# Kernel optimization log

Measured on AMD Instinct MI355X. Metric: run time of the kernel, lower is better.

The kernel has to match this reference:

```python
import jax, jax.numpy as jnp
import numpy as np

N, E, D_NODE, D_EDGE, H, NUM_CLASSES = 2048, 4096, 128, 128, 4, 16
SPARSE_RATIO = 0.5  # forward arg sparse_ratio; <1.0 triggers top-k node masking
NEG = jnp.float32(-1e9)


def _mha(x, wq, bq, wk, bk, wv, bv, wo, bo, mask):
    """Multi-head self-attention over tokens x [T, D]; mask broadcastable to [H, T, T]."""
    T, D = x.shape
    dh = D // H
    q = (x @ wq + bq).reshape(T, H, dh)
    k = (x @ wk + bk).reshape(T, H, dh)
    v = (x @ wv + bv).reshape(T, H, dh)
    scores = jnp.einsum('qhd,khd->hqk', q, k) * (1.0 / float(np.sqrt(dh)))
    scores = jnp.where(mask, scores, NEG)
    attn = jax.nn.softmax(scores, axis=-1)
    out = jnp.einsum('hqk,khd->qhd', attn, v).reshape(T, D)
    return out @ wo + bo


def setup_inputs() -> dict:
    key = jax.random.key(0)
    ks = jax.random.split(key, 20)
    f32 = jnp.float32
    def w(i, shape):
        return jax.random.normal(ks[i], shape, dtype=f32) * 0.02
    z = lambda *s: jnp.zeros(s, f32)
    return {
        'node_features': jax.random.normal(ks[0], (N, D_NODE), dtype=f32),
        'edge_features': jax.random.normal(ks[1], (E, D_EDGE), dtype=f32),
        'edge_index': jax.random.randint(ks[2], (2, E), 0, N),
        'w_rn': w(3, (D_NODE, 1)), 'b_rn': z(1),
        'w_re': w(4, (D_EDGE, 1)), 'b_re': z(1),
        'wq_n': w(5, (D_NODE, D_NODE)), 'bq_n': z(D_NODE),
        'wk_n': w(6, (D_NODE, D_NODE)), 'bk_n': z(D_NODE),
        'wv_n': w(7, (D_NODE, D_NODE)), 'bv_n': z(D_NODE),
        'wo_n': w(8, (D_NODE, D_NODE)), 'bo_n': z(D_NODE),
        'wq_e': w(9, (D_EDGE, D_EDGE)), 'bq_e': z(D_EDGE),
        'wk_e': w(10, (D_EDGE, D_EDGE)), 'bk_e': z(D_EDGE),
        'wv_e': w(11, (D_EDGE, D_EDGE)), 'bv_e': z(D_EDGE),
        'wo_e': w(12, (D_EDGE, D_EDGE)), 'bo_e': z(D_EDGE),
        'w_ne': w(13, (D_NODE, D_EDGE)), 'b_ne': z(D_EDGE),
        'w_c1': w(14, (D_EDGE, 2 * D_EDGE)), 'b_c1': z(2 * D_EDGE),
        'w_c2': w(15, (2 * D_EDGE, NUM_CLASSES)), 'b_c2': z(NUM_CLASSES),
    }


def reference(node_features, edge_features, edge_index,
              w_rn, b_rn, w_re, b_re,
              wq_n, bq_n, wk_n, bk_n, wv_n, bv_n, wo_n, bo_n,
              wq_e, bq_e, wk_e, bk_e, wv_e, bv_e, wo_e, bo_e,
              w_ne, b_ne, w_c1, b_c1, w_c2, b_c2):
    # Importance router: scalar sigmoid scores per node / edge
    node_scores = jax.nn.sigmoid(node_features @ w_rn + b_rn)[:, 0]  # [N]
    edge_scores = jax.nn.sigmoid(edge_features @ w_re + b_re)[:, 0]  # [E]
    # Gate features by importance (routing)
    x_n = node_features * node_scores[:, None]
    x_e = edge_features * edge_scores[:, None]
    # Conditional top-k node mask (sparse_ratio < 1.0)
    k = int(SPARSE_RATIO * N)
    thresh = jax.lax.top_k(node_scores, k)[0][-1]
    node_mask = node_scores >= thresh  # [N] bool, keys kept in node attention
    # Edge adjacency (line graph): edges sharing an endpoint attend to each other
    src, dst = edge_index[0], edge_index[1]
    adj = ((src[:, None] == src[None, :]) | (src[:, None] == dst[None, :]) |
           (dst[:, None] == src[None, :]) | (dst[:, None] == dst[None, :]))  # [E, E]
    # Dual parallel attention
    node_out = _mha(x_n, wq_n, bq_n, wk_n, bk_n, wv_n, bv_n, wo_n, bo_n,
                    node_mask[None, None, :])
    edge_out = _mha(x_e, wq_e, bq_e, wk_e, bk_e, wv_e, bv_e, wo_e, bo_e,
                    adj[None, :, :])
    node_msg = node_out[src] + node_out[dst]  # [E, D_NODE] gather at endpoints
    updated_edges = edge_out + node_msg @ w_ne + b_ne  # [E, D_EDGE]
    # Classifier: Linear -> GELU -> Linear
    h = jax.nn.gelu(updated_edges @ w_c1 + b_c1)
    return h @ w_c2 + b_c2  # [E, NUM_CLASSES]
```

## Files before the change

### kernel.cpp

```cpp
#include <hip/hip_runtime.h>
#include <math.h>

#define N_NODES 2048
#define N_EDGES 4096
#define DIM 128
#define HEADS 4
#define DH 32
#define NCLS 16
#define TOPK 1024
#define NBR_CAP 64
#define NSPLIT 4
#define QB 32
#define SCALE 0.17677669529663687f

#define FMA4(ACC, AS, BV)                                       \
  ACC.x = fmaf(AS, BV.x, ACC.x); ACC.y = fmaf(AS, BV.y, ACC.y); \
  ACC.z = fmaf(AS, BV.z, ACC.z); ACC.w = fmaf(AS, BV.w, ACC.w)

__device__ __forceinline__ float wave_reduce_sum(float v) {
#pragma unroll
  for (int o = 32; o > 0; o >>= 1) v += __shfl_xor(v, o, 64);
  return v;
}

__global__ __launch_bounds__(256) void prep_kernel(
    const float* __restrict__ nf, const float* __restrict__ ef,
    const float* __restrict__ w_rn, const float* __restrict__ b_rn,
    const float* __restrict__ w_re, const float* __restrict__ b_re,
    const int* __restrict__ src, const int* __restrict__ dst,
    const float* __restrict__ wo_n, const float* __restrict__ bo_n,
    const float* __restrict__ w_ne, const float* __restrict__ b_ne,
    float* __restrict__ ns, float* __restrict__ es, int* __restrict__ nbr,
    int* __restrict__ deg, float* __restrict__ wfu, float* __restrict__ bfu) {
  int tid = threadIdx.x;
  int bid = blockIdx.x;
  if (bid < 1536) {
    int wid = tid >> 6, lane = tid & 63;
    int row = bid * 4 + wid;
    const float* feat;
    const float* w;
    float b;
    float* scp;
    if (row < N_NODES) {
      feat = nf + (size_t)row * DIM;
      w = w_rn; b = b_rn[0];
      scp = ns + row;
    } else {
      int r = row - N_NODES;
      feat = ef + (size_t)r * DIM;
      w = w_re; b = b_re[0];
      scp = es + r;
    }
    float d = feat[lane] * w[lane] + feat[lane + 64] * w[lane + 64];
    d = wave_reduce_sum(d);
    if (lane == 0) *scp = 1.0f / (1.0f + __expf(-(d + b)));
    return;
  }
  if (bid < 2048) {
    __shared__ int sL[N_EDGES];
    __shared__ int dL[N_EDGES];
    __shared__ int cnt[8];
    int bq = bid - 1536;
#pragma unroll
    for (int i = 0; i < 16; i++) {
      int j = i * 256 + tid;
      sL[j] = src[j];
      dL[j] = dst[j];
    }
    if (tid < 8) cnt[tid] = 0;
    __syncthreads();
    int w = tid >> 6, lane = tid & 63;
#pragma unroll
    for (int qq = 0; qq < 2; qq++) {
      int slot = w * 2 + qq;
      int qi = bq * 8 + slot;
      int sq = sL[qi], dq = dL[qi];
      for (int j = lane; j < N_EDGES; j += 64) {
        int sj = sL[j], dj = dL[j];
        if (sj == sq || sj == dq || dj == sq || dj == dq) {
          int pos = atomicAdd(&cnt[slot], 1);
          if (pos < NBR_CAP) nbr[(size_t)qi * NBR_CAP + pos] = j;
        }
      }
    }
    __syncthreads();
    if (tid < 8) deg[bq * 8 + tid] = min(cnt[tid], NBR_CAP);
    return;
  }
  if (bid < 2052) {
    __shared__ float As[16][68];
    __shared__ float Bs[16][68];
    int idx = bid - 2048;
    int bm = (idx >> 1) * 64, bn = (idx & 1) * 64;
    int tm = (tid >> 4) * 4, tn = (tid & 15) * 4;
    float4 acc[4] = {{0,0,0,0},{0,0,0,0},{0,0,0,0},{0,0,0,0}};
    for (int k0 = 0; k0 < DIM; k0 += 16) {
#pragma unroll
      for (int i = 0; i < 4; i++) {
        int e = i * 256 + tid;
        int r = e >> 4, kk = e & 15;
        As[kk][r] = wo_n[(size_t)(bm + r) * DIM + k0 + kk];
        int kb = e >> 6, c = e & 63;
        Bs[kb][c] = w_ne[(size_t)(k0 + kb) * DIM + bn + c];
      }
      __syncthreads();
#pragma unroll
      for (int kk = 0; kk < 16; kk++) {
        float4 a = *(const float4*)&As[kk][tm];
        float4 b = *(const float4*)&Bs[kk][tn];
        FMA4(acc[0], a.x, b); FMA4(acc[1], a.y, b);
        FMA4(acc[2], a.z, b); FMA4(acc[3], a.w, b);
      }
      __syncthreads();
    }
#pragma unroll
    for (int i = 0; i < 4; i++)
      *(float4*)&wfu[(size_t)(bm + tm + i) * DIM + bn + tn] = acc[i];
    return;
  }
  if (tid < DIM) {
    float a = 0.f;
    for (int k = 0; k < DIM; k++)
      a = fmaf(bo_n[k], w_ne[(size_t)k * DIM + tid], a);
    bfu[tid] = 2.f * a + b_ne[tid];
  }
}

typedef float As128T[16][136];
typedef float Bs68T[16][68];
__device__ __forceinline__ void gemm_body128(
    As128T& As, Bs68T& Bs, const float* __restrict__ A,
    const float* __restrict__ B, const float* gs, int bm, int bn, int K,
    int N, float4 (&acc)[8], int tid) {
  int g4 = (tid >> 4) * 4, tn = (tid & 15) * 4;
  for (int k0 = 0; k0 < K; k0 += 16) {
#pragma unroll
    for (int i = 0; i < 8; i++) {
      int e = i * 256 + tid;
      int r = e >> 4, kk = e & 15;
      float a = A[(size_t)(bm + r) * K + k0 + kk];
      As[kk][r] = gs ? a * gs[r] : a;
    }
#pragma unroll
    for (int i = 0; i < 4; i++) {
      int e = i * 256 + tid;
      int kb = e >> 6, c = e & 63;
      Bs[kb][c] = B[(size_t)(k0 + kb) * N + bn + c];
    }
    __syncthreads();
#pragma unroll
    for (int kk = 0; kk < 16; kk++) {
      float4 a0 = *(const float4*)&As[kk][g4];
      float4 a1 = *(const float4*)&As[kk][g4 + 64];
      float4 b = *(const float4*)&Bs[kk][tn];
      FMA4(acc[0], a0.x, b); FMA4(acc[1], a0.y, b);
      FMA4(acc[2], a0.z, b); FMA4(acc[3], a0.w, b);
      FMA4(acc[4], a1.x, b); FMA4(acc[5], a1.y, b);
      FMA4(acc[6], a1.z, b); FMA4(acc[7], a1.w, b);
    }
    __syncthreads();
  }
}

__global__ __launch_bounds__(256) void topk_qkv_kernel(
    const float* __restrict__ nf, const float* __restrict__ ef,
    const float* __restrict__ ns, const float* __restrict__ es,
    const float* __restrict__ wq_n, const float* __restrict__ wk_n,
    const float* __restrict__ wv_n, const float* __restrict__ wq_e,
    const float* __restrict__ wk_e, const float* __restrict__ wv_e,
    const float* __restrict__ bq_n, const float* __restrict__ bk_n,
    const float* __restrict__ bv_n, const float* __restrict__ bq_e,
    const float* __restrict__ bk_e, const float* __restrict__ bv_e,
    float* __restrict__ qn, float* __restrict__ kn, float* __restrict__ vn,
    float* __restrict__ qe, float* __restrict__ ke, float* __restrict__ ve,
    int* __restrict__ kidx, int* __restrict__ nkept) {
  __shared__ float As[16][136];
  __shared__ float Bs[16][68];
  __shared__ float ss[128];
  __shared__ unsigned sh_lo;
  __shared__ int wcnt;
  int tid = threadIdx.x;
  if (blockIdx.x == 0) {
    if (tid == 0) wcnt = 0;
    if (tid < 64) {
      unsigned bv[32];
#pragma unroll
      for (int i = 0; i < 32; i++) bv[i] = __float_as_uint(ns[tid * 32 + i]);
      unsigned lo = 0u, hi = 0x3F800000u;
      while (lo < hi) {
        unsigned mid = (unsigned)(((unsigned long long)lo + hi + 1ull) >> 1);
        int c = 0;
#pragma unroll
        for (int i = 0; i < 32; i++) c += (bv[i] >= mid);
#pragma unroll
        for (int o = 1; o < 64; o <<= 1) c += __shfl_xor(c, o, 64);
        if (c >= TOPK) lo = mid; else hi = mid - 1;
      }
      if (tid == 0) sh_lo = lo;
    }
    __syncthreads();
    unsigned lo = sh_lo;
#pragma unroll
    for (int i = 0; i < 8; i++) {
      int idx = tid * 8 + i;
      if (__float_as_uint(ns[idx]) >= lo) kidx[atomicAdd(&wcnt, 1)] = idx;
    }
    __syncthreads();
    if (tid == 0) nkept[0] = wcnt;
    return;
  }
  int bx = blockIdx.x - 1;
  bool edge = bx >= 96;
  int mat, bm, bn;
  const float* A;
  const float* sc;
  if (!edge) {
    mat = bx / 32;
    int rem = bx % 32;
    bm = (rem >> 1) * 128;
    bn = (rem & 1) * 64;
    A = nf; sc = ns;
  } else {
    int be = bx - 96;
    mat = be / 64;
    int rem = be % 64;
    bm = (rem >> 1) * 128;
    bn = (rem & 1) * 64;
    A = ef; sc = es;
  }
  const float* W;
  const float* bias;
  float* C;
  if (!edge) {
    if (mat == 0) { W = wq_n; bias = bq_n; C = qn; }
    else if (mat == 1) { W = wk_n; bias = bk_n; C = kn; }
    else { W = wv_n; bias = bv_n; C = vn; }
  } else {
    if (mat == 0) { W = wq_e; bias = bq_e; C = qe; }
    else if (mat == 1) { W = wk_e; bias = bk_e; C = ke; }
    else { W = wv_e; bias = bv_e; C = ve; }
  }
  if (tid < 128) ss[tid] = sc[bm + tid];
  __syncthreads();
  float4 acc[8] = {{0,0,0,0},{0,0,0,0},{0,0,0,0},{0,0,0,0},
                   {0,0,0,0},{0,0,0,0},{0,0,0,0},{0,0,0,0}};
  gemm_body128(As, Bs, A, W, ss, bm, bn, DIM, DIM, acc, tid);
  int g4 = (tid >> 4) * 4, tn = (tid & 15) * 4;
  float4 b4 = *(const float4*)&bias[bn + tn];
#pragma unroll
  for (int i = 0; i < 4; i++) {
    float4 r;
    r.x = acc[i].x + b4.x; r.y = acc[i].y + b4.y;
    r.z = acc[i].z + b4.z; r.w = acc[i].w + b4.w;
    *(float4*)&C[(size_t)(bm + g4 + i) * DIM + bn + tn] = r;
  }
#pragma unroll
  for (int i = 0; i < 4; i++) {
    float4 r;
    r.x = acc[4 + i].x + b4.x; r.y = acc[4 + i].y + b4.y;
    r.z = acc[4 + i].z + b4.z; r.w = acc[4 + i].w + b4.w;
    *(float4*)&C[(size_t)(bm + 64 + g4 + i) * DIM + bn + tn] = r;
  }
}

__global__ __launch_bounds__(256) void attn_kernel(
    const float* __restrict__ Q, const float* __restrict__ K,
    const float* __restrict__ V, const int* __restrict__ kidx,
    const int* __restrict__ nkeptp, float* __restrict__ pacc,
    float* __restrict__ ps,
    const float* __restrict__ Qe, const float* __restrict__ Ke,
    const float* __restrict__ Ve, const int* __restrict__ nbr,
    const int* __restrict__ deg, float* __restrict__ Oe) {
  __shared__ float Qs[32][36];
  __shared__ float Ks[64][36];
  __shared__ float Vs[64][36];
  __shared__ float Ps[32][68];
  int tid = threadIdx.x;
  int bid = blockIdx.x;
  if (bid < 1024) {
    int bxa = bid & 63;
    int h = (bid >> 6) & 3;
    int sp = bid >> 8;
    int qbase = bxa * QB;
    int nkept = nkeptp[0];
    int spl = (nkept + NSPLIT - 1) / NSPLIT;
    int start = sp * spl;
    int end = min(start + spl, nkept);

    {
      int q8 = tid >> 3, d8 = tid & 7;
      const float4* qp =
          (const float4*)(Q + (size_t)(qbase + q8) * DIM + h * DH) + d8;
      float4 qv = *qp;
      Qs[d8 * 4 + 0][q8] = qv.x;
      Qs[d8 * 4 + 1][q8] = qv.y;
      Qs[d8 * 4 + 2][q8] = qv.z;
      Qs[d8 * 4 + 3][q8] = qv.w;
    }

    int tq = tid >> 5;
    int tk = tid & 31;
    float o[4] = {0.f, 0.f, 0.f, 0.f};
    float sump[4] = {0.f, 0.f, 0.f, 0.f};

    for (int t0 = start; t0 < end; t0 += 64) {
#pragma unroll
      for (int i = 0; i < 2; i++) {
        int id = i * 256 + tid;
        int r = id >> 3, c4 = id & 7;
        int row = t0 + r;
        int ki = (row < end) ? kidx[row] : kidx[0];
        const float4* kp = (const float4*)(K + (size_t)ki * DIM + h * DH) + c4;
        const float4* vp = (const float4*)(V + (size_t)ki * DIM + h * DH) + c4;
        *(float4*)&Ks[r][c4 * 4] = *kp;
        *(float4*)&Vs[r][c4 * 4] = *vp;
      }
      __syncthreads();
      float4 s0v = {0.f, 0.f, 0.f, 0.f};
      float4 s1v = {0.f, 0.f, 0.f, 0.f};
#pragma unroll
      for (int kk4 = 0; kk4 < 8; kk4++) {
        int kk = kk4 * 4;
        float4 ka = *(const float4*)&Ks[tk][kk];
        float4 kb = *(const float4*)&Ks[tk + 32][kk];
        float4 qa = *(const float4*)&Qs[kk + 0][tq * 4];
        float4 qb = *(const float4*)&Qs[kk + 1][tq * 4];
        float4 qc = *(const float4*)&Qs[kk + 2][tq * 4];
        float4 qd = *(const float4*)&Qs[kk + 3][tq * 4];
        FMA4(s0v, ka.x, qa); FMA4(s0v, ka.y, qb);
        FMA4(s0v, ka.z, qc); FMA4(s0v, ka.w, qd);
        FMA4(s1v, kb.x, qa); FMA4(s1v, kb.y, qb);
        FMA4(s1v, kb.z, qc); FMA4(s1v, kb.w, qd);
      }
      bool va = (t0 + tk) < end;
      bool vb = (t0 + tk + 32) < end;
      float p00 = va ? __expf(s0v.x * SCALE) : 0.f;
      float p01 = va ? __expf(s0v.y * SCALE) : 0.f;
      float p02 = va ? __expf(s0v.z * SCALE) : 0.f;
      float p03 = va ? __expf(s0v.w * SCALE) : 0.f;
      float p10 = vb ? __expf(s1v.x * SCALE) : 0.f;
      float p11 = vb ? __expf(s1v.y * SCALE) : 0.f;
      float p12 = vb ? __expf(s1v.z * SCALE) : 0.f;
      float p13 = vb ? __expf(s1v.w * SCALE) : 0.f;
      Ps[tq * 4 + 0][tk] = p00;      Ps[tq * 4 + 1][tk] = p01;
      Ps[tq * 4 + 2][tk] = p02;      Ps[tq * 4 + 3][tk] = p03;
      Ps[tq * 4 + 0][tk + 32] = p10; Ps[tq * 4 + 1][tk + 32] = p11;
      Ps[tq * 4 + 2][tk + 32] = p12; Ps[tq * 4 + 3][tk + 32] = p13;
      sump[0] += p00 + p10;
      sump[1] += p01 + p11;
      sump[2] += p02 + p12;
      sump[3] += p03 + p13;
      __syncthreads();
#pragma unroll
      for (int k4 = 0; k4 < 16; k4++) {
        int k = k4 * 4;
        float4 p0 = *(const float4*)&Ps[tq * 4 + 0][k];
        float4 p1 = *(const float4*)&Ps[tq * 4 + 1][k];
        float4 p2 = *(const float4*)&Ps[tq * 4 + 2][k];
        float4 p3 = *(const float4*)&Ps[tq * 4 + 3][k];
        float w0 = Vs[k + 0][tk], w1 = Vs[k + 1][tk];
        float w2 = Vs[k + 2][tk], w3 = Vs[k + 3][tk];
        o[0] = fmaf(p0.x, w0, o[0]); o[0] = fmaf(p0.y, w1, o[0]);
        o[0] = fmaf(p0.z, w2, o[0]); o[0] = fmaf(p0.w, w3, o[0]);
        o[1] = fmaf(p1.x, w0, o[1]); o[1] = fmaf(p1.y, w1, o[1]);
        o[1] = fmaf(p1.z, w2, o[1]); o[1] = fmaf(p1.w, w3, o[1]);
        o[2] = fmaf(p2.x, w0, o[2]); o[2] = fmaf(p2.y, w1, o[2]);
        o[2] = fmaf(p2.z, w2, o[2]); o[2] = fmaf(p2.w, w3, o[2]);
        o[3] = fmaf(p3.x, w0, o[3]); o[3] = fmaf(p3.y, w1, o[3]);
        o[3] = fmaf(p3.z, w2, o[3]); o[3] = fmaf(p3.w, w3, o[3]);
      }
      __syncthreads();
    }
#pragma unroll
    for (int os = 1; os < 32; os <<= 1) {
#pragma unroll
      for (int j = 0; j < 4; j++) sump[j] += __shfl_xor(sump[j], os, 64);
    }
#pragma unroll
    for (int j = 0; j < 4; j++) {
      int q = qbase + tq * 4 + j;
      size_t idx = ((size_t)q * HEADS + h) * NSPLIT + sp;
      pacc[idx * 32 + tk] = o[j];
      if (tk == 0) ps[idx] = sump[j];
    }
    return;
  }
  int h = tid >> 6;
  int lane = tid & 63;
  int ql = lane >> 4, j4 = (lane >> 2) & 3, g = lane & 3;
  int qi = (bid - 1024) * 4 + ql;
  int dg = deg[qi];
  const float4* qp = (const float4*)(Qe + (size_t)qi * DIM + h * DH + g * 8);
  float4 q0 = qp[0], q1 = qp[1];
  float s = 0.f;
  float4 a0 = make_float4(0.f, 0.f, 0.f, 0.f);
  float4 a1 = make_float4(0.f, 0.f, 0.f, 0.f);
  for (int c0 = 0; c0 < dg; c0 += 4) {
    int j = c0 + j4;
    bool act = j < dg;
    int ei = act ? nbr[(size_t)qi * NBR_CAP + j] : 0;
    const float4* kp = (const float4*)(Ke + (size_t)ei * DIM + h * DH + g * 8);
    float4 k0 = kp[0], k1 = kp[1];
    float pd = q0.x * k0.x + q0.y * k0.y + q0.z * k0.z + q0.w * k0.w +
               q1.x * k1.x + q1.y * k1.y + q1.z * k1.z + q1.w * k1.w;
    pd += __shfl_xor(pd, 1, 64);
    pd += __shfl_xor(pd, 2, 64);
    float pr = act ? __expf(pd * SCALE) : 0.f;
    s += pr;
    const float4* vp = (const float4*)(Ve + (size_t)ei * DIM + h * DH + g * 8);
    float4 v0 = vp[0], v1 = vp[1];
    FMA4(a0, pr, v0);
    FMA4(a1, pr, v1);
  }
#pragma unroll
  for (int o = 4; o <= 8; o <<= 1) {
    s += __shfl_xor(s, o, 64);
    a0.x += __shfl_xor(a0.x, o, 64); a0.y += __shfl_xor(a0.y, o, 64);
    a0.z += __shfl_xor(a0.z, o, 64); a0.w += __shfl_xor(a0.w, o, 64);
    a1.x += __shfl_xor(a1.x, o, 64); a1.y += __shfl_xor(a1.y, o, 64);
    a1.z += __shfl_xor(a1.z, o, 64); a1.w += __shfl_xor(a1.w, o, 64);
  }
  if (j4 == 0) {
    float inv = 1.0f / s;
    float4* op = (float4*)(Oe + (size_t)qi * DIM + h * DH + g * 8);
    float4 r0 = {a0.x * inv, a0.y * inv, a0.z * inv, a0.w * inv};
    float4 r1 = {a1.x * inv, a1.y * inv, a1.z * inv, a1.w * inv};
    op[0] = r0;
    op[1] = r1;
  }
}

__global__ __launch_bounds__(256) void attn_reduce_kernel(
    const float* __restrict__ pacc, const float* __restrict__ ps,
    float* __restrict__ O) {
  int gid = blockIdx.x * 256 + threadIdx.x;
  int qh = gid >> 5, d = gid & 31;
  int q = qh >> 2, h = qh & 3;
  float ssum = 0.f, v = 0.f;
#pragma unroll
  for (int sp = 0; sp < NSPLIT; sp++) {
    size_t idx = (size_t)qh * NSPLIT + sp;
    ssum += ps[idx];
    v += pacc[idx * 32 + d];
  }
  O[(size_t)q * DIM + h * DH + d] = v / ssum;
}

__global__ __launch_bounds__(256) void tail_kernel(
    const float* __restrict__ aoe, const float* __restrict__ wo_e,
    const float* __restrict__ bo_e, const float* __restrict__ aon,
    const int* __restrict__ src, const int* __restrict__ dst,
    const float* __restrict__ wfu, const float* __restrict__ bfu,
    const float* __restrict__ w_c1, const float* __restrict__ b_c1,
    float* __restrict__ hb) {
  __shared__ __align__(16) char smem[25344];
  float (*ue_s)[132] = (float(*)[132])smem;
  float (*As0)[20] = (float(*)[20])(smem + 8448);
  float (*Bs)[132] = (float(*)[132])(smem + 9728);
  float (*Bs2)[264] = (float(*)[264])(smem + 8448);
  int tid = threadIdx.x;
  int bm = blockIdx.x * 16;
  int tmr = (tid >> 5) * 2;
  int tn = (tid & 31) * 4;
  float4 acc[2] = {{0,0,0,0},{0,0,0,0}};
  for (int k0 = 0; k0 < DIM; k0 += 16) {
    {
      int r = tid >> 4, kk = tid & 15;
      As0[kk][r] = aoe[(size_t)(bm + r) * DIM + k0 + kk];
    }
#pragma unroll
    for (int i = 0; i < 8; i++) {
      int id = i * 256 + tid;
      int kb = id >> 7, c = id & 127;
      Bs[kb][c] = wo_e[(size_t)(k0 + kb) * DIM + c];
    }
    __syncthreads();
#pragma unroll
    for (int kk = 0; kk < 16; kk++) {
      float2 a = *(const float2*)&As0[kk][tmr];
      float4 b = *(const float4*)&Bs[kk][tn];
      FMA4(acc[0], a.x, b);
      FMA4(acc[1], a.y, b);
    }
    __syncthreads();
  }
  for (int k0 = 0; k0 < DIM; k0 += 16) {
    {
      int r = tid >> 4, kk = tid & 15;
      int row = bm + r;
      int s0 = src[row], d0 = dst[row];
      As0[kk][r] = aon[(size_t)s0 * DIM + k0 + kk] +
                   aon[(size_t)d0 * DIM + k0 + kk];
    }
#pragma unroll
    for (int i = 0; i < 8; i++) {
      int id = i * 256 + tid;
      int kb = id >> 7, c = id & 127;
      Bs[kb][c] = wfu[(size_t)(k0 + kb) * DIM + c];
    }
    __syncthreads();
#pragma unroll
    for (int kk = 0; kk < 16; kk++) {
      float2 a = *(const float2*)&As0[kk][tmr];
      float4 b = *(const float4*)&Bs[kk][tn];
      FMA4(acc[0], a.x, b);
      FMA4(acc[1], a.y, b);
    }
    __syncthreads();
  }
  {
    float4 be = *(const float4*)&bo_e[tn];
    float4 bf = *(const float4*)&bfu[tn];
#pragma unroll
    for (int i = 0; i < 2; i++) {
      float4 r;
      r.x = acc[i].x + be.x + bf.x; r.y = acc[i].y + be.y + bf.y;
      r.z = acc[i].z + be.z + bf.z; r.w = acc[i].w + be.w + bf.w;
      *(float4*)&ue_s[tmr + i][tn] = r;
    }
  }
  __syncthreads();
  int c4 = (tid & 31) * 4;
  float4 acc2[2][2] = {{{0,0,0,0},{0,0,0,0}},{{0,0,0,0},{0,0,0,0}}};
  for (int k0 = 0; k0 < DIM; k0 += 16) {
#pragma unroll
    for (int i = 0; i < 16; i++) {
      int id = i * 256 + tid;
      int kb = id >> 8, c = id & 255;
      Bs2[kb][c] = w_c1[(size_t)(k0 + kb) * 256 + c];
    }
    __syncthreads();
#pragma unroll
    for (int kk = 0; kk < 16; kk++) {
      float a0v = ue_s[tmr][k0 + kk];
      float a1v = ue_s[tmr + 1][k0 + kk];
      float4 bva = *(const float4*)&Bs2[kk][c4];
      float4 bvb = *(const float4*)&Bs2[kk][c4 + 128];
      FMA4(acc2[0][0], a0v, bva); FMA4(acc2[0][1], a0v, bvb);
      FMA4(acc2[1][0], a1v, bva); FMA4(acc2[1][1], a1v, bvb);
    }
    __syncthreads();
  }
  float4 bc0 = *(const float4*)&b_c1[c4];
  float4 bc1 = *(const float4*)&b_c1[c4 + 128];
#pragma unroll
  for (int i = 0; i < 2; i++) {
#pragma unroll
    for (int half = 0; half < 2; half++) {
      float4 bb = half ? bc1 : bc0;
      float vv[4] = {acc2[i][half].x + bb.x, acc2[i][half].y + bb.y,
                     acc2[i][half].z + bb.z, acc2[i][half].w + bb.w};
#pragma unroll
      for (int j = 0; j < 4; j++) {
        float v = vv[j];
        float u = 0.7978845608028654f * (v + 0.044715f * v * v * v);
        vv[j] = 0.5f * v * (1.0f + tanhf(u));
      }
      float4 r = {vv[0], vv[1], vv[2], vv[3]};
      *(float4*)&hb[(size_t)(bm + tmr + i) * 256 + c4 + half * 128] = r;
    }
  }
}

__global__ __launch_bounds__(256) void gemm_out_kernel(
    const float* __restrict__ Hm, const float* __restrict__ B,
    const float* __restrict__ bias, float* __restrict__ C) {
  __shared__ float Bs[256 * 16];
  int tid = threadIdx.x;
#pragma unroll
  for (int i = 0; i < 16; i++) Bs[i * 256 + tid] = B[i * 256 + tid];
  __syncthreads();
  int row = blockIdx.x * 16 + (tid >> 4);
  int col = tid & 15;
  const float* hp = Hm + (size_t)row * 256;
  float sacc = bias[col];
#pragma unroll 8
  for (int k = 0; k < 256; k++) sacc = fmaf(hp[k], Bs[k * 16 + col], sacc);
  C[(size_t)row * NCLS + col] = sacc;
}

extern "C" void kernel_launch(void* const* d_in, const int* in_sizes, int n_in,
                              void* d_out, int out_size, void* d_ws,
                              size_t ws_size, hipStream_t stream) {
  const float* nf = (const float*)d_in[0];
  const float* ef = (const float*)d_in[1];
  const int* ei = (const int*)d_in[2];
  const float* w_rn = (const float*)d_in[3];
  const float* b_rn = (const float*)d_in[4];
  const float* w_re = (const float*)d_in[5];
  const float* b_re = (const float*)d_in[6];
  const float* wq_n = (const float*)d_in[7];
  const float* bq_n = (const float*)d_in[8];
  const float* wk_n = (const float*)d_in[9];
  const float* bk_n = (const float*)d_in[10];
  const float* wv_n = (const float*)d_in[11];
  const float* bv_n = (const float*)d_in[12];
  const float* wo_n = (const float*)d_in[13];
  const float* bo_n = (const float*)d_in[14];
  const float* wq_e = (const float*)d_in[15];
  const float* bq_e = (const float*)d_in[16];
  const float* wk_e = (const float*)d_in[17];
  const float* bk_e = (const float*)d_in[18];
  const float* wv_e = (const float*)d_in[19];
  const float* bv_e = (const float*)d_in[20];
  const float* wo_e = (const float*)d_in[21];
  const float* bo_e = (const float*)d_in[22];
  const float* w_ne = (const float*)d_in[23];
  const float* b_ne = (const float*)d_in[24];
  const float* w_c1 = (const float*)d_in[25];
  const float* b_c1 = (const float*)d_in[26];
  const float* w_c2 = (const float*)d_in[27];
  const float* b_c2 = (const float*)d_in[28];

  const int* src = ei;
  const int* dst = ei + N_EDGES;

  float* ws = (float*)d_ws;
  size_t o = 0;
  float* ns = ws + o;   o += 2048;
  float* es = ws + o;   o += 4096;
  int* kidx = (int*)(ws + o); o += 2048;
  int* nkept = (int*)(ws + o); o += 64;
  int* nbr = (int*)(ws + o); o += (size_t)N_EDGES * NBR_CAP;
  int* degp = (int*)(ws + o); o += N_EDGES;
  float* wfu = ws + o;  o += DIM * DIM;
  float* bfu = ws + o;  o += DIM;
  float* qn = ws + o;   o += (size_t)N_NODES * DIM;
  float* kn = ws + o;   o += (size_t)N_NODES * DIM;
  float* vn = ws + o;   o += (size_t)N_NODES * DIM;
  float* qe = ws + o;   o += (size_t)N_EDGES * DIM;
  float* ke = ws + o;   o += (size_t)N_EDGES * DIM;
  float* ve = ws + o;   o += (size_t)N_EDGES * DIM;
  float* aon = ws + o;  o += (size_t)N_NODES * DIM;
  float* aoe = ws + o;  o += (size_t)N_EDGES * DIM;
  float* hb = ws + o;   o += (size_t)N_EDGES * 2 * DIM;
  float* ps = ws + o;   o += (size_t)N_NODES * HEADS * NSPLIT;
  float* pacc = hb;

  prep_kernel<<<dim3(2053), 256, 0, stream>>>(
      nf, ef, w_rn, b_rn, w_re, b_re, src, dst, wo_n, bo_n, w_ne, b_ne,
      ns, es, nbr, degp, wfu, bfu);
  topk_qkv_kernel<<<dim3(289), 256, 0, stream>>>(
      nf, ef, ns, es, wq_n, wk_n, wv_n, wq_e, wk_e, wv_e,
      bq_n, bk_n, bv_n, bq_e, bk_e, bv_e, qn, kn, vn, qe, ke, ve,
      kidx, nkept);
  attn_kernel<<<dim3(2048), 256, 0, stream>>>(
      qn, kn, vn, kidx, nkept, pacc, ps, qe, ke, ve, nbr, degp, aoe);
  attn_reduce_kernel<<<dim3(N_NODES * HEADS * DH / 256), 256, 0, stream>>>(
      pacc, ps, aon);
  tail_kernel<<<dim3(N_EDGES / 16), 256, 0, stream>>>(
      aoe, wo_e, bo_e, aon, src, dst, wfu, bfu, w_c1, b_c1, hb);
  gemm_out_kernel<<<dim3(N_EDGES / 16), 256, 0, stream>>>(hb, w_c2, b_c2,
                                                          (float*)d_out);
}
```

Measured before the change: 115.3 us.

## Increase block counts and split work in neighbor build, attention PV, tail, output GEMM

The line-graph neighbor builder now handles 4 query edges per block instead of 8, doubling its block count. The node attention P·V step splits the key dimension across four thread groups with float4 V reads, then reduces the partial outputs through shared memory. The tail and output GEMM kernels process 8 rows per block instead of 16, and the output GEMM splits K across two halves with a shared-memory reduction. All of this aims to raise parallelism and occupancy, at the cost of extra syncs, reductions and redundant loads of src/dst and weights.

```diff
diff --git a/kernel.cpp b/kernel.cpp
--- a/kernel.cpp
+++ b/kernel.cpp
@@ -56,10 +56,10 @@
     if (lane == 0) *scp = 1.0f / (1.0f + __expf(-(d + b)));
     return;
   }
-  if (bid < 2048) {
+  if (bid < 2560) {
     __shared__ int sL[N_EDGES];
     __shared__ int dL[N_EDGES];
-    __shared__ int cnt[8];
+    __shared__ int cnt[4];
     int bq = bid - 1536;
 #pragma unroll
     for (int i = 0; i < 16; i++) {
@@ -67,30 +67,26 @@
       sL[j] = src[j];
       dL[j] = dst[j];
     }
-    if (tid < 8) cnt[tid] = 0;
+    if (tid < 4) cnt[tid] = 0;
     __syncthreads();
     int w = tid >> 6, lane = tid & 63;
-#pragma unroll
-    for (int qq = 0; qq < 2; qq++) {
-      int slot = w * 2 + qq;
-      int qi = bq * 8 + slot;
-      int sq = sL[qi], dq = dL[qi];
-      for (int j = lane; j < N_EDGES; j += 64) {
-        int sj = sL[j], dj = dL[j];
-        if (sj == sq || sj == dq || dj == sq || dj == dq) {
-          int pos = atomicAdd(&cnt[slot], 1);
-          if (pos < NBR_CAP) nbr[(size_t)qi * NBR_CAP + pos] = j;
-        }
-      }
-    }
-    __syncthreads();
-    if (tid < 8) deg[bq * 8 + tid] = min(cnt[tid], NBR_CAP);
+    int qi = bq * 4 + w;
+    int sq = sL[qi], dq = dL[qi];
+    for (int j = lane; j < N_EDGES; j += 64) {
+      int sj = sL[j], dj = dL[j];
+      if (sj == sq || sj == dq || dj == sq || dj == dq) {
+        int pos = atomicAdd(&cnt[w], 1);
+        if (pos < NBR_CAP) nbr[(size_t)qi * NBR_CAP + pos] = j;
+      }
+    }
+    __syncthreads();
+    if (tid < 4) deg[bq * 4 + tid] = min(cnt[tid], NBR_CAP);
     return;
   }
-  if (bid < 2052) {
+  if (bid < 2564) {
     __shared__ float As[16][68];
     __shared__ float Bs[16][68];
-    int idx = bid - 2048;
+    int idx = bid - 2560;
     int bm = (idx >> 1) * 64, bn = (idx & 1) * 64;
     int tm = (tid >> 4) * 4, tn = (tid & 15) * 4;
     float4 acc[4] = {{0,0,0,0},{0,0,0,0},{0,0,0,0},{0,0,0,0}};
@@ -300,7 +296,10 @@
 
     int tq = tid >> 5;
     int tk = tid & 31;
-    float o[4] = {0.f, 0.f, 0.f, 0.f};
+    int kg = tid >> 6;
+    int tq2 = (tid >> 3) & 7;
+    int td4 = tid & 7;
+    float4 o4[4] = {{0,0,0,0},{0,0,0,0},{0,0,0,0},{0,0,0,0}};
     float sump[4] = {0.f, 0.f, 0.f, 0.f};
 
     for (int t0 = start; t0 < end; t0 += 64) {
@@ -352,22 +351,24 @@
       sump[3] += p03 + p13;
       __syncthreads();
 #pragma unroll
-      for (int k4 = 0; k4 < 16; k4++) {
-        int k = k4 * 4;
-        float4 p0 = *(const float4*)&Ps[tq * 4 + 0][k];
-        float4 p1 = *(const float4*)&Ps[tq * 4 + 1][k];
-        float4 p2 = *(const float4*)&Ps[tq * 4 + 2][k];
-        float4 p3 = *(const float4*)&Ps[tq * 4 + 3][k];
-        float w0 = Vs[k + 0][tk], w1 = Vs[k + 1][tk];
-        float w2 = Vs[k + 2][tk], w3 = Vs[k + 3][tk];
-        o[0] = fmaf(p0.x, w0, o[0]); o[0] = fmaf(p0.y, w1, o[0]);
-        o[0] = fmaf(p0.z, w2, o[0]); o[0] = fmaf(p0.w, w3, o[0]);
-        o[1] = fmaf(p1.x, w0, o[1]); o[1] = fmaf(p1.y, w1, o[1]);
-        o[1] = fmaf(p1.z, w2, o[1]); o[1] = fmaf(p1.w, w3, o[1]);
-        o[2] = fmaf(p2.x, w0, o[2]); o[2] = fmaf(p2.y, w1, o[2]);
-        o[2] = fmaf(p2.z, w2, o[2]); o[2] = fmaf(p2.w, w3, o[2]);
-        o[3] = fmaf(p3.x, w0, o[3]); o[3] = fmaf(p3.y, w1, o[3]);
-        o[3] = fmaf(p3.z, w2, o[3]); o[3] = fmaf(p3.w, w3, o[3]);
+      for (int k4 = 0; k4 < 4; k4++) {
+        int kb = kg * 16 + k4 * 4;
+        float4 p0 = *(const float4*)&Ps[tq2 * 4 + 0][kb];
+        float4 p1 = *(const float4*)&Ps[tq2 * 4 + 1][kb];
+        float4 p2 = *(const float4*)&Ps[tq2 * 4 + 2][kb];
+        float4 p3 = *(const float4*)&Ps[tq2 * 4 + 3][kb];
+        float4 v0 = *(const float4*)&Vs[kb + 0][td4 * 4];
+        float4 v1 = *(const float4*)&Vs[kb + 1][td4 * 4];
+        float4 v2 = *(const float4*)&Vs[kb + 2][td4 * 4];
+        float4 v3 = *(const float4*)&Vs[kb + 3][td4 * 4];
+        FMA4(o4[0], p0.x, v0); FMA4(o4[0], p0.y, v1);
+        FMA4(o4[0], p0.z, v2); FMA4(o4[0], p0.w, v3);
+        FMA4(o4[1], p1.x, v0); FMA4(o4[1], p1.y, v1);
+        FMA4(o4[1], p1.z, v2); FMA4(o4[1], p1.w, v3);
+        FMA4(o4[2], p2.x, v0); FMA4(o4[2], p2.y, v1);
+        FMA4(o4[2], p2.z, v2); FMA4(o4[2], p2.w, v3);
+        FMA4(o4[3], p3.x, v0); FMA4(o4[3], p3.y, v1);
+        FMA4(o4[3], p3.z, v2); FMA4(o4[3], p3.w, v3);
       }
       __syncthreads();
     }
@@ -376,12 +377,37 @@
 #pragma unroll
       for (int j = 0; j < 4; j++) sump[j] += __shfl_xor(sump[j], os, 64);
     }
-#pragma unroll
-    for (int j = 0; j < 4; j++) {
-      int q = qbase + tq * 4 + j;
-      size_t idx = ((size_t)q * HEADS + h) * NSPLIT + sp;
-      pacc[idx * 32 + tk] = o[j];
-      if (tk == 0) ps[idx] = sump[j];
+    if (tk == 0) {
+#pragma unroll
+      for (int j = 0; j < 4; j++) {
+        int q = qbase + tq * 4 + j;
+        size_t idx = ((size_t)q * HEADS + h) * NSPLIT + sp;
+        ps[idx] = sump[j];
+      }
+    }
+    float* scrA = &Ks[0][0];
+    float* scrB = &Vs[0][0];
+    int slot = (kg * 64 + tq2 * 8 + td4) * 8;
+    *(float4*)&scrA[slot + 0] = o4[0];
+    *(float4*)&scrA[slot + 4] = o4[1];
+    *(float4*)&scrB[slot + 0] = o4[2];
+    *(float4*)&scrB[slot + 4] = o4[3];
+    __syncthreads();
+    {
+      int qq = tid >> 3;
+      int d4 = tid & 7;
+      int tqr = qq >> 2, j = qq & 3;
+      const float* bank = (j < 2) ? scrA : scrB;
+      int off = (j & 1) * 4;
+      float4 of = {0.f, 0.f, 0.f, 0.f};
+#pragma unroll
+      for (int g = 0; g < 4; g++) {
+        float4 part =
+            *(const float4*)&bank[(g * 64 + tqr * 8 + d4) * 8 + off];
+        of.x += part.x; of.y += part.y; of.z += part.z; of.w += part.w;
+      }
+      size_t idx = ((size_t)(qbase + qq) * HEADS + h) * NSPLIT + sp;
+      *(float4*)&pacc[idx * 32 + d4 * 4] = of;
     }
     return;
   }
@@ -453,18 +479,18 @@
     const float* __restrict__ wfu, const float* __restrict__ bfu,
     const float* __restrict__ w_c1, const float* __restrict__ b_c1,
     float* __restrict__ hb) {
-  __shared__ __align__(16) char smem[25344];
+  __shared__ __align__(16) char smem[21120];
   float (*ue_s)[132] = (float(*)[132])smem;
-  float (*As0)[20] = (float(*)[20])(smem + 8448);
-  float (*Bs)[132] = (float(*)[132])(smem + 9728);
-  float (*Bs2)[264] = (float(*)[264])(smem + 8448);
+  float (*As0)[12] = (float(*)[12])(smem + 4224);
+  float (*Bs)[132] = (float(*)[132])(smem + 4992);
+  float (*Bs2)[264] = (float(*)[264])(smem + 4224);
   int tid = threadIdx.x;
-  int bm = blockIdx.x * 16;
-  int tmr = (tid >> 5) * 2;
+  int bm = blockIdx.x * 8;
+  int tr = tid >> 5;
   int tn = (tid & 31) * 4;
-  float4 acc[2] = {{0,0,0,0},{0,0,0,0}};
+  float4 acc = {0, 0, 0, 0};
   for (int k0 = 0; k0 < DIM; k0 += 16) {
-    {
+    if (tid < 128) {
       int r = tid >> 4, kk = tid & 15;
       As0[kk][r] = aoe[(size_t)(bm + r) * DIM + k0 + kk];
     }
@@ -477,15 +503,14 @@
     __syncthreads();
 #pragma unroll
     for (int kk = 0; kk < 16; kk++) {
-      float2 a = *(const float2*)&As0[kk][tmr];
+      float a = As0[kk][tr];
       float4 b = *(const float4*)&Bs[kk][tn];
-      FMA4(acc[0], a.x, b);
-      FMA4(acc[1], a.y, b);
+      FMA4(acc, a, b);
     }
     __syncthreads();
   }
   for (int k0 = 0; k0 < DIM; k0 += 16) {
-    {
+    if (tid < 128) {
       int r = tid >> 4, kk = tid & 15;
       int row = bm + r;
       int s0 = src[row], d0 = dst[row];
@@ -501,27 +526,23 @@
     __syncthreads();
 #pragma unroll
     for (int kk = 0; kk < 16; kk++) {
-      float2 a = *(const float2*)&As0[kk][tmr];
+      float a = As0[kk][tr];
       float4 b = *(const float4*)&Bs[kk][tn];
-      FMA4(acc[0], a.x, b);
-      FMA4(acc[1], a.y, b);
+      FMA4(acc, a, b);
     }
     __syncthreads();
   }
   {
     float4 be = *(const float4*)&bo_e[tn];
     float4 bf = *(const float4*)&bfu[tn];
-#pragma unroll
-    for (int i = 0; i < 2; i++) {
-      float4 r;
-      r.x = acc[i].x + be.x + bf.x; r.y = acc[i].y + be.y + bf.y;
-      r.z = acc[i].z + be.z + bf.z; r.w = acc[i].w + be.w + bf.w;
-      *(float4*)&ue_s[tmr + i][tn] = r;
-    }
+    float4 r;
+    r.x = acc.x + be.x + bf.x; r.y = acc.y + be.y + bf.y;
+    r.z = acc.z + be.z + bf.z; r.w = acc.w + be.w + bf.w;
+    *(float4*)&ue_s[tr][tn] = r;
   }
   __syncthreads();
   int c4 = (tid & 31) * 4;
-  float4 acc2[2][2] = {{{0,0,0,0},{0,0,0,0}},{{0,0,0,0},{0,0,0,0}}};
+  float4 acc2[2] = {{0,0,0,0},{0,0,0,0}};
   for (int k0 = 0; k0 < DIM; k0 += 16) {
 #pragma unroll
     for (int i = 0; i < 16; i++) {
@@ -532,33 +553,29 @@
     __syncthreads();
 #pragma unroll
     for (int kk = 0; kk < 16; kk++) {
-      float a0v = ue_s[tmr][k0 + kk];
-      float a1v = ue_s[tmr + 1][k0 + kk];
+      float av = ue_s[tr][k0 + kk];
       float4 bva = *(const float4*)&Bs2[kk][c4];
       float4 bvb = *(const float4*)&Bs2[kk][c4 + 128];
-      FMA4(acc2[0][0], a0v, bva); FMA4(acc2[0][1], a0v, bvb);
-      FMA4(acc2[1][0], a1v, bva); FMA4(acc2[1][1], a1v, bvb);
+      FMA4(acc2[0], av, bva);
+      FMA4(acc2[1], av, bvb);
     }
     __syncthreads();
   }
   float4 bc0 = *(const float4*)&b_c1[c4];
   float4 bc1 = *(const float4*)&b_c1[c4 + 128];
 #pragma unroll
-  for (int i = 0; i < 2; i++) {
-#pragma unroll
-    for (int half = 0; half < 2; half++) {
-      float4 bb = half ? bc1 : bc0;
-      float vv[4] = {acc2[i][half].x + bb.x, acc2[i][half].y + bb.y,
-                     acc2[i][half].z + bb.z, acc2[i][half].w + bb.w};
-#pragma unroll
-      for (int j = 0; j < 4; j++) {
-        float v = vv[j];
-        float u = 0.7978845608028654f * (v + 0.044715f * v * v * v);
-        vv[j] = 0.5f * v * (1.0f + tanhf(u));
-      }
-      float4 r = {vv[0], vv[1], vv[2], vv[3]};
-      *(float4*)&hb[(size_t)(bm + tmr + i) * 256 + c4 + half * 128] = r;
-    }
+  for (int half = 0; half < 2; half++) {
+    float4 bb = half ? bc1 : bc0;
+    float4 av = acc2[half];
+    float vv[4] = {av.x + bb.x, av.y + bb.y, av.z + bb.z, av.w + bb.w};
+#pragma unroll
+    for (int j = 0; j < 4; j++) {
+      float v = vv[j];
+      float u = 0.7978845608028654f * (v + 0.044715f * v * v * v);
+      vv[j] = 0.5f * v * (1.0f + tanhf(u));
+    }
+    float4 r = {vv[0], vv[1], vv[2], vv[3]};
+    *(float4*)&hb[(size_t)(bm + tr) * 256 + c4 + half * 128] = r;
   }
 }
 
@@ -566,17 +583,23 @@
     const float* __restrict__ Hm, const float* __restrict__ B,
     const float* __restrict__ bias, float* __restrict__ C) {
   __shared__ float Bs[256 * 16];
+  __shared__ float red[256];
   int tid = threadIdx.x;
 #pragma unroll
   for (int i = 0; i < 16; i++) Bs[i * 256 + tid] = B[i * 256 + tid];
   __syncthreads();
-  int row = blockIdx.x * 16 + (tid >> 4);
+  int row = blockIdx.x * 8 + ((tid >> 4) & 7);
   int col = tid & 15;
-  const float* hp = Hm + (size_t)row * 256;
-  float sacc = bias[col];
+  int half = tid >> 7;
+  const float* hp = Hm + (size_t)row * 256 + half * 128;
+  float sacc = half ? 0.f : bias[col];
 #pragma unroll 8
-  for (int k = 0; k < 256; k++) sacc = fmaf(hp[k], Bs[k * 16 + col], sacc);
-  C[(size_t)row * NCLS + col] = sacc;
+  for (int k = 0; k < 128; k++)
+    sacc = fmaf(hp[k], Bs[(half * 128 + k) * 16 + col], sacc);
+  red[tid] = sacc;
+  __syncthreads();
+  if (tid < 128)
+    C[(size_t)row * NCLS + col] = red[tid] + red[tid + 128];
 }
 
 extern "C" void kernel_launch(void* const* d_in, const int* in_sizes, int n_in,
@@ -637,7 +660,7 @@
   float* ps = ws + o;   o += (size_t)N_NODES * HEADS * NSPLIT;
   float* pacc = hb;
 
-  prep_kernel<<<dim3(2053), 256, 0, stream>>>(
+  prep_kernel<<<dim3(2565), 256, 0, stream>>>(
       nf, ef, w_rn, b_rn, w_re, b_re, src, dst, wo_n, bo_n, w_ne, b_ne,
       ns, es, nbr, degp, wfu, bfu);
   topk_qkv_kernel<<<dim3(289), 256, 0, stream>>>(
@@ -648,8 +671,8 @@
       qn, kn, vn, kidx, nkept, pacc, ps, qe, ke, ve, nbr, degp, aoe);
   attn_reduce_kernel<<<dim3(N_NODES * HEADS * DH / 256), 256, 0, stream>>>(
       pacc, ps, aon);
-  tail_kernel<<<dim3(N_EDGES / 16), 256, 0, stream>>>(
+  tail_kernel<<<dim3(N_EDGES / 8), 256, 0, stream>>>(
       aoe, wo_e, bo_e, aon, src, dst, wfu, bfu, w_c1, b_c1, hb);
-  gemm_out_kernel<<<dim3(N_EDGES / 16), 256, 0, stream>>>(hb, w_c2, b_c2,
-                                                          (float*)d_out);
-}
+  gemm_out_kernel<<<dim3(N_EDGES / 8), 256, 0, stream>>>(hb, w_c2, b_c2,
+                                                         (float*)d_out);
+}
```

Measured after the change: 108.1 us. -6.3%, faster.
